# Optimization experiments

Hardware: AMD Instinct MI355X
Metric: run time of the kernel (lower is better)

The kernel has to match this reference:

```python
import jax, jax.numpy as jnp
import numpy as np

N, E, F_IN = 10000, 160000, 256
H1, C1 = 8, 128          # conv1: heads=8, out 128 per head, concat -> 1024
H2, C2 = 1, 64           # conv2: heads=1, out 64
NEG_SLOPE = 0.2


def setup_inputs() -> dict:
    key = jax.random.key(0)
    ks = jax.random.split(key, 10)
    s_in = 1.0 / np.sqrt(F_IN)
    s_h1 = 1.0 / np.sqrt(H1 * C1)
    return {
        "x": jax.random.normal(ks[0], (N, F_IN), dtype=jnp.float32),
        "edge_index": jax.random.randint(ks[1], (2, E), 0, N, dtype=jnp.int64),
        "W1": jax.random.normal(ks[2], (F_IN, H1 * C1), dtype=jnp.float32) * s_in,
        "att_src1": jax.random.normal(ks[3], (H1, C1), dtype=jnp.float32) * 0.1,
        "att_dst1": jax.random.normal(ks[4], (H1, C1), dtype=jnp.float32) * 0.1,
        "b1": jnp.zeros((H1 * C1,), dtype=jnp.float32),
        "W2": jax.random.normal(ks[5], (H1 * C1, H2 * C2), dtype=jnp.float32) * s_h1,
        "att_src2": jax.random.normal(ks[6], (H2, C2), dtype=jnp.float32) * 0.1,
        "att_dst2": jax.random.normal(ks[7], (H2, C2), dtype=jnp.float32) * 0.1,
        "b2": jnp.zeros((H2 * C2,), dtype=jnp.float32),
    }


def gat_conv(x, src, dst, W, att_src, att_dst, b, n):
    """PyG GATConv (eval mode: dropout off), concat=True, add_self_loops handled by caller."""
    H, C = att_src.shape
    h = (x @ W).reshape(n, H, C)                       # [N,H,C]
    a_s = jnp.einsum('nhc,hc->nh', h, att_src)         # [N,H]
    a_d = jnp.einsum('nhc,hc->nh', h, att_dst)         # [N,H]
    e = jax.nn.leaky_relu(a_s[src] + a_d[dst], NEG_SLOPE)  # [Etot,H]
    # softmax over edges grouped by destination node (numerically stable)
    e_max = jax.ops.segment_max(e, dst, num_segments=n)
    e = jnp.exp(e - e_max[dst])
    denom = jax.ops.segment_sum(e, dst, num_segments=n)
    alpha = e / (denom[dst] + 1e-16)                   # [Etot,H]
    msg = h[src] * alpha[:, :, None]                   # [Etot,H,C]
    out = jax.ops.segment_sum(msg, dst, num_segments=n)  # [N,H,C]
    return out.reshape(n, H * C) + b


def reference(x, edge_index, W1, att_src1, att_dst1, b1, W2, att_src2, att_dst2, b2):
    n = x.shape[0]
    loops = jnp.arange(n, dtype=edge_index.dtype)
    src = jnp.concatenate([edge_index[0], loops])
    dst = jnp.concatenate([edge_index[1], loops])
    h = jax.nn.elu(gat_conv(x, src, dst, W1, att_src1, att_dst1, b1, n))
    return gat_conv(h, src, dst, W2, att_src2, att_dst2, b2, n)
```

## Files before the change

### kernel.cpp

```cpp
#include <hip/hip_runtime.h>
#include <cmath>


typedef _Float16 f16x8 __attribute__((ext_vector_type(8)));
typedef float f32x4 __attribute__((ext_vector_type(4)));
typedef unsigned short u16x8 __attribute__((ext_vector_type(8)));

__device__ __forceinline__ float lrelu(float x) { return x > 0.f ? x : 0.2f * x; }
__device__ __forceinline__ unsigned short f2h(float f) {
  _Float16 h = (_Float16)f;
  return __builtin_bit_cast(unsigned short, h);
}
__device__ __forceinline__ float h2f(unsigned short u) {
  return (float)__builtin_bit_cast(_Float16, u);
}

__device__ __forceinline__ void fma8h(float* acc, uint4 v, float e) {
  acc[0] += e * h2f((unsigned short)(v.x & 0xffffu));
  acc[1] += e * h2f((unsigned short)(v.x >> 16));
  acc[2] += e * h2f((unsigned short)(v.y & 0xffffu));
  acc[3] += e * h2f((unsigned short)(v.y >> 16));
  acc[4] += e * h2f((unsigned short)(v.z & 0xffffu));
  acc[5] += e * h2f((unsigned short)(v.z >> 16));
  acc[6] += e * h2f((unsigned short)(v.w & 0xffffu));
  acc[7] += e * h2f((unsigned short)(v.w >> 16));
}

#define GLOAD_LDS16(gsrc, ldst)                                              \
  __builtin_amdgcn_global_load_lds(                                          \
      (const __attribute__((address_space(1))) unsigned int*)(gsrc),         \
      (__attribute__((address_space(3))) unsigned int*)(ldst), 16, 0, 0)


__global__ __launch_bounds__(256) void prep_fused(
    const int* __restrict__ ei, int* __restrict__ counts, int E,
    const float* __restrict__ x, unsigned short* __restrict__ xpk, int N, int MB1,
    const float* __restrict__ W1, unsigned short* __restrict__ w1pk,
    const float* __restrict__ W2, unsigned short* __restrict__ w2pk) {
  const int countB = (E + 255) / 256;
  const int pxB = MB1 * 8;
  int bid = blockIdx.x;
  int t = threadIdx.x;

  if (bid < countB) {
    int e = bid * 256 + t;
    if (e < E) atomicAdd(&counts[ei[E + e]], 1);
    return;
  }
  bid -= countB;
  if (bid < pxB) {
    int mb = bid >> 3, ks = bid & 7;
    int l = t & 63, f = t >> 6;
    int row = mb * 64 + f * 16 + (l & 15);
    int kc = ks * 32 + (l >> 4) * 8;
    float v[8];
#pragma unroll
    for (int j = 0; j < 8; ++j) v[j] = 0.f;
    if (row < N) {
      const float* xr = x + (size_t)row * 256 + kc;
#pragma unroll
      for (int j = 0; j < 8; ++j) v[j] = xr[j];
    }
    u16x8 hv;
#pragma unroll
    for (int j = 0; j < 8; ++j) hv[j] = f2h(v[j]);
    size_t base = (size_t)(mb * 8 + ks) * 2048;
    *(u16x8*)(xpk + base + (size_t)f * 512 + l * 8) = hv;
    return;
  }
  bid -= pxB;
  if (bid < 64) {
    int hb = bid >> 3, ks = bid & 7;
    int l = t & 63, gq = t >> 6;
    for (int g = gq; g < 8; g += 4) {
      int n = hb * 128 + g * 16 + (l & 15);
      int k0 = ks * 32 + (l >> 4) * 8;
      u16x8 hv;
#pragma unroll
      for (int j = 0; j < 8; ++j) hv[j] = f2h(W1[(size_t)(k0 + j) * 1024 + n]);
      size_t base = (size_t)(hb * 8 + ks) * 4096;
      *(u16x8*)(w1pk + base + (size_t)g * 512 + l * 8) = hv;
    }
    return;
  }
  bid -= 64;
  {
    int ks = bid;
    int l = t & 63, g = t >> 6;
    int n = g * 16 + (l & 15);
    int k0 = ks * 32 + (l >> 4) * 8;
    u16x8 hv;
#pragma unroll
    for (int j = 0; j < 8; ++j) hv[j] = f2h(W2[(size_t)(k0 + j) * 64 + n]);
    size_t base = (size_t)ks * 2048;
    *(u16x8*)(w2pk + base + (size_t)g * 512 + l * 8) = hv;
  }
}


__global__ __launch_bounds__(256) void scan_blk(const int* __restrict__ counts,
                                                int* __restrict__ offsets,
                                                int* __restrict__ bsum, int n) {
  __shared__ int lds[256];
  int b = blockIdx.x, t = threadIdx.x, i = b * 256 + t;
  int v = (i < n) ? counts[i] + 1 : 0;
  lds[t] = v;
  __syncthreads();
  for (int off = 1; off < 256; off <<= 1) {
    int tv = (t >= off) ? lds[t - off] : 0;
    __syncthreads();
    lds[t] += tv;
    __syncthreads();
  }
  if (i < n) offsets[i] = lds[t] - v;
  if (t == 255) bsum[b] = lds[255];
}

__global__ __launch_bounds__(256) void scan_apply(int* __restrict__ offsets,
                                                  int* __restrict__ cursors,
                                                  const int* __restrict__ bsum,
                                                  int nb, int n) {
  __shared__ int pre_s;
  int b = blockIdx.x, t = threadIdx.x;
  if (t == 0) {
    int s = 0;
    for (int i = 0; i < b; ++i) s += bsum[i];
    pre_s = s;
    if (b == nb - 1) {
      int tot = s;
      for (int i = b; i < nb; ++i) tot += bsum[i];
      offsets[n] = tot;
    }
  }
  __syncthreads();
  int i = b * 256 + t;
  if (i < n) {
    int o = offsets[i] + pre_s;
    offsets[i] = o;
    cursors[i] = o;
  }
}

__global__ __launch_bounds__(256) void fill_all(const int* __restrict__ ei,
                                                int* __restrict__ cursors,
                                                const int* __restrict__ offsets,
                                                int* __restrict__ list,
                                                int E, int n) {
  int tid = blockIdx.x * 256 + threadIdx.x;
  if (tid < E) {
    int d = ei[E + tid];
    int pos = atomicAdd(&cursors[d], 1);
    list[pos] = ei[tid];
  } else if (tid < E + n) {
    int i = tid - E;
    list[offsets[i + 1] - 1] = i;
  }
}


__global__ __launch_bounds__(512, 4) void gemm1_att(
    const unsigned short* __restrict__ xpk, const unsigned short* __restrict__ w1pk,
    const float* __restrict__ asrc, const float* __restrict__ adst,
    unsigned short* __restrict__ h1b, float* __restrict__ as1,
    float* __restrict__ ad1) {
  extern __shared__ char sm[];
  const int t = threadIdx.x, wid = t >> 6, lane = t & 63;
  const int wr = wid >> 2, wc = wid & 3;
  const int mb = blockIdx.x, hb = blockIdx.y;
  const int m0 = mb * 128;
  const int l15 = lane & 15, l4 = lane >> 4;

  f32x4 acc[4][2] = {};

  auto stage = [&](int buf, int ks) {
    char* base0 = sm + buf * 16384;
    for (int i = wid; i < 16; i += 8) {
      const unsigned short* src;
      int ldsoff;
      if (i < 8) {
        int r = i >> 2;
        src = xpk + (size_t)((2 * mb + r) * 8 + ks) * 2048 + (i & 3) * 512 + lane * 8;
        ldsoff = i * 1024;
      } else {
        int g = i - 8;
        src = w1pk + (size_t)(hb * 8 + ks) * 4096 + g * 512 + lane * 8;
        ldsoff = 8192 + g * 1024;
      }
      GLOAD_LDS16(src, base0 + ldsoff);
    }
  };

  stage(0, 0);
  __syncthreads();
  int buf = 0;
  for (int step = 0; step < 8; ++step) {
    if (step < 7) stage(buf ^ 1, step + 1);
    const char* b = sm + buf * 16384;
    f16x8 ah[4], bh[2];
#pragma unroll
    for (int mf = 0; mf < 4; ++mf)
      ah[mf] = *(const f16x8*)(b + (wr * 4 + mf) * 1024 + lane * 16);
#pragma unroll
    for (int nf = 0; nf < 2; ++nf)
      bh[nf] = *(const f16x8*)(b + 8192 + (wc * 2 + nf) * 1024 + lane * 16);
#pragma unroll
    for (int mf = 0; mf < 4; ++mf)
#pragma unroll
      for (int nf = 0; nf < 2; ++nf)
        acc[mf][nf] = __builtin_amdgcn_mfma_f32_16x16x32_f16(ah[mf], bh[nf], acc[mf][nf], 0, 0, 0);
    __syncthreads();
    buf ^= 1;
  }

  float* parts_s = (float*)sm;
  float* parts_d = (float*)(sm + 2048);
  unsigned short* ctile = (unsigned short*)(sm + 4096);
  float as_c[2], ad_c[2];
#pragma unroll
  for (int nf = 0; nf < 2; ++nf) {
    int col = hb * 128 + wc * 32 + nf * 16 + l15;
    as_c[nf] = asrc[col];
    ad_c[nf] = adst[col];
  }
#pragma unroll
  for (int mf = 0; mf < 4; ++mf) {
    float ss[4] = {0.f, 0.f, 0.f, 0.f}, dd[4] = {0.f, 0.f, 0.f, 0.f};
#pragma unroll
    for (int nf = 0; nf < 2; ++nf)
#pragma unroll
      for (int r = 0; r < 4; ++r) {
        ss[r] += acc[mf][nf][r] * as_c[nf];
        dd[r] += acc[mf][nf][r] * ad_c[nf];
      }
#pragma unroll
    for (int r = 0; r < 4; ++r)
      for (int m = 1; m < 16; m <<= 1) {
        ss[r] += __shfl_xor(ss[r], m);
        dd[r] += __shfl_xor(dd[r], m);
      }
    if (l15 == 0) {
#pragma unroll
      for (int r = 0; r < 4; ++r) {
        int row = wr * 64 + mf * 16 + l4 * 4 + r;
        parts_s[row * 4 + wc] = ss[r];
        parts_d[row * 4 + wc] = dd[r];
      }
    }
#pragma unroll
    for (int nf = 0; nf < 2; ++nf)
#pragma unroll
      for (int r = 0; r < 4; ++r) {
        int row = wr * 64 + mf * 16 + l4 * 4 + r;
        int col = wc * 32 + nf * 16 + l15;
        ctile[row * 128 + col] = f2h(acc[mf][nf][r]);
      }
  }
  __syncthreads();
  if (t < 128) {
    float s = parts_s[t * 4] + parts_s[t * 4 + 1] + parts_s[t * 4 + 2] + parts_s[t * 4 + 3];
    float d = parts_d[t * 4] + parts_d[t * 4 + 1] + parts_d[t * 4 + 2] + parts_d[t * 4 + 3];
    as1[(size_t)(m0 + t) * 8 + hb] = s;
    ad1[(size_t)(m0 + t) * 8 + hb] = d;
  }
#pragma unroll
  for (int rep = 0; rep < 4; ++rep) {
    int e = rep * 4096 + t * 8;
    int row = e >> 7, col = e & 127;
    u16x8 v = *(const u16x8*)(ctile + e);
    *(u16x8*)(h1b + (size_t)(m0 + row) * 1024 + hb * 128 + col) = v;
  }
}


__global__ __launch_bounds__(256) void agg1_gather(
    const unsigned short* __restrict__ h1b, const float* __restrict__ as1,
    const float* __restrict__ ad1, const int* __restrict__ offsets,
    const int* __restrict__ list, const float* __restrict__ b1,
    unsigned short* __restrict__ o1pk, int n, int nblk) {
  __shared__ __align__(16) unsigned short stg[4096];
  const int t = threadIdx.x, w = t >> 6, lane = t & 63;
  const int h0 = lane >> 4, h1_ = h0 + 4;

  for (int blk = blockIdx.x; blk < nblk; blk += gridDim.x) {
    const int node = blk * 4 + w;
    if (node < n) {
      const int beg = offsets[node], end = offsets[node + 1];
      const float ad0 = ad1[(size_t)node * 8 + h0];
      const float ad4 = ad1[(size_t)node * 8 + h1_];
      float acc0[8] = {}, acc1[8] = {};
      float den0 = 0.f, den4 = 0.f;

      int j = beg;
      int sA = 0, sB = 0;
      float aA0 = 0.f, aA4 = 0.f, aB0 = 0.f, aB4 = 0.f;
      uint4 vA0, vA1, vB0, vB1;
      if (j + 2 <= end) {
        sA = list[j]; sB = list[j + 1];
        aA0 = as1[(size_t)sA * 8 + h0]; aA4 = as1[(size_t)sA * 8 + h1_];
        aB0 = as1[(size_t)sB * 8 + h0]; aB4 = as1[(size_t)sB * 8 + h1_];
        vA0 = *(const uint4*)(h1b + (size_t)sA * 1024 + lane * 8);
        vA1 = *(const uint4*)(h1b + (size_t)sA * 1024 + 512 + lane * 8);
        vB0 = *(const uint4*)(h1b + (size_t)sB * 1024 + lane * 8);
        vB1 = *(const uint4*)(h1b + (size_t)sB * 1024 + 512 + lane * 8);
      }
      for (; j + 4 <= end; j += 2) {
        int sA2 = list[j + 2], sB2 = list[j + 3];
        float aA02 = as1[(size_t)sA2 * 8 + h0], aA42 = as1[(size_t)sA2 * 8 + h1_];
        float aB02 = as1[(size_t)sB2 * 8 + h0], aB42 = as1[(size_t)sB2 * 8 + h1_];
        uint4 nA0 = *(const uint4*)(h1b + (size_t)sA2 * 1024 + lane * 8);
        uint4 nA1 = *(const uint4*)(h1b + (size_t)sA2 * 1024 + 512 + lane * 8);
        uint4 nB0 = *(const uint4*)(h1b + (size_t)sB2 * 1024 + lane * 8);
        uint4 nB1 = *(const uint4*)(h1b + (size_t)sB2 * 1024 + 512 + lane * 8);
        float eA0 = __expf(lrelu(aA0 + ad0)), eA4 = __expf(lrelu(aA4 + ad4));
        float eB0 = __expf(lrelu(aB0 + ad0)), eB4 = __expf(lrelu(aB4 + ad4));
        den0 += eA0 + eB0; den4 += eA4 + eB4;
        fma8h(acc0, vA0, eA0); fma8h(acc1, vA1, eA4);
        fma8h(acc0, vB0, eB0); fma8h(acc1, vB1, eB4);
        sA = sA2; sB = sB2;
        aA0 = aA02; aA4 = aA42; aB0 = aB02; aB4 = aB42;
        vA0 = nA0; vA1 = nA1; vB0 = nB0; vB1 = nB1;
      }
      if (j + 2 <= end) {
        float eA0 = __expf(lrelu(aA0 + ad0)), eA4 = __expf(lrelu(aA4 + ad4));
        float eB0 = __expf(lrelu(aB0 + ad0)), eB4 = __expf(lrelu(aB4 + ad4));
        den0 += eA0 + eB0; den4 += eA4 + eB4;
        fma8h(acc0, vA0, eA0); fma8h(acc1, vA1, eA4);
        fma8h(acc0, vB0, eB0); fma8h(acc1, vB1, eB4);
        j += 2;
      }
      if (j < end) {
        int s = list[j];
        float a0 = as1[(size_t)s * 8 + h0], a4 = as1[(size_t)s * 8 + h1_];
        uint4 v0 = *(const uint4*)(h1b + (size_t)s * 1024 + lane * 8);
        uint4 v1 = *(const uint4*)(h1b + (size_t)s * 1024 + 512 + lane * 8);
        float e0 = __expf(lrelu(a0 + ad0)), e4 = __expf(lrelu(a4 + ad4));
        den0 += e0; den4 += e4;
        fma8h(acc0, v0, e0); fma8h(acc1, v1, e4);
      }

      const float inv0 = 1.f / (den0 + 1e-16f);
      const float inv4 = 1.f / (den4 + 1e-16f);
      u16x8 hA8, hB8;
#pragma unroll
      for (int k = 0; k < 8; ++k) {
        float vA = acc0[k] * inv0 + b1[lane * 8 + k];
        float vB = acc1[k] * inv4 + b1[512 + lane * 8 + k];
        vA = vA > 0.f ? vA : expm1f(vA);
        vB = vB > 0.f ? vB : expm1f(vB);
        hA8[k] = f2h(vA);
        hB8[k] = f2h(vB);
      }
      const int q2 = lane >> 2, kc = lane & 3;
      {
        int aw = q2 * 256 + kc * 64 + w * 16;
        *(u16x8*)((char*)stg + (aw ^ ((q2 & 7) << 4))) = hA8;
      }
      {
        int ks = 16 + q2;
        int aw = ks * 256 + kc * 64 + w * 16;
        *(u16x8*)((char*)stg + (aw ^ ((ks & 7) << 4))) = hB8;
      }
    }
    __syncthreads();
    const int mb = blk >> 4, f = (blk >> 2) & 3, l15b = (blk & 3) * 4;
#pragma unroll
    for (int it = 0; it < 2; ++it) {
      int a = it * 4096 + t * 16;
      int ks = a >> 8, kcc = (a >> 6) & 3, ww = (a >> 4) & 3;
      u16x8 v = *(const u16x8*)((const char*)stg + (a ^ ((ks & 7) << 4)));
      size_t g = (size_t)(mb * 32 + ks) * 2048 + (size_t)f * 512 +
                 (size_t)(kcc * 16 + l15b + ww) * 8;
      *(u16x8*)(o1pk + g) = v;
    }
    __syncthreads();
  }
}


__global__ __launch_bounds__(256) void gemm2_splitk(
    const unsigned short* __restrict__ o1pk, const unsigned short* __restrict__ w2pk,
    float* __restrict__ h2p, int Mpad) {
  extern __shared__ char sm[];
  const int t = threadIdx.x, wid = t >> 6, lane = t & 63;
  const int wr = wid >> 1, wc = wid & 1;
  const int mb = blockIdx.x, sk = blockIdx.y;
  const int m0 = mb * 64;
  const int l15 = lane & 15, l4 = lane >> 4;

  f32x4 acc[2][2] = {};

  auto stage = [&](int buf, int ks) {
    char* base0 = sm + buf * 8192;
    const unsigned short* ax = o1pk + (size_t)(mb * 32 + ks) * 2048 + lane * 8;
    for (int i = wid; i < 4; i += 4)
      GLOAD_LDS16(ax + i * 512, base0 + i * 1024);
    if (wid >= 0) {
      int i = wid;
      GLOAD_LDS16(ax + i * 512, base0 + i * 1024);
      const unsigned short* bw = w2pk + (size_t)ks * 2048 + lane * 8;
      GLOAD_LDS16(bw + i * 512, base0 + 4096 + i * 1024);
    }
  };

  stage(0, sk * 8);
  __syncthreads();
  int buf = 0;
  for (int step = 0; step < 8; ++step) {
    if (step < 7) stage(buf ^ 1, sk * 8 + step + 1);
    const char* b = sm + buf * 8192;
    f16x8 ah[2], bh[2];
#pragma unroll
    for (int mf = 0; mf < 2; ++mf)
      ah[mf] = *(const f16x8*)(b + (wr * 2 + mf) * 1024 + lane * 16);
#pragma unroll
    for (int nf = 0; nf < 2; ++nf)
      bh[nf] = *(const f16x8*)(b + 4096 + (wc * 2 + nf) * 1024 + lane * 16);
#pragma unroll
    for (int mf = 0; mf < 2; ++mf)
#pragma unroll
      for (int nf = 0; nf < 2; ++nf)
        acc[mf][nf] = __builtin_amdgcn_mfma_f32_16x16x32_f16(ah[mf], bh[nf], acc[mf][nf], 0, 0, 0);
    __syncthreads();
    buf ^= 1;
  }

#pragma unroll
  for (int mf = 0; mf < 2; ++mf)
#pragma unroll
    for (int nf = 0; nf < 2; ++nf)
#pragma unroll
      for (int r = 0; r < 4; ++r) {
        int row = wr * 32 + mf * 16 + l4 * 4 + r;
        int col = wc * 32 + nf * 16 + l15;
        h2p[((size_t)sk * Mpad + m0 + row) * 64 + col] = acc[mf][nf][r];
      }
}


__global__ __launch_bounds__(256) void reduce_att2(
    const float* __restrict__ h2p, const float* __restrict__ asrc,
    const float* __restrict__ adst, float* __restrict__ h2,
    float* __restrict__ as2, float* __restrict__ ad2, int Mpad, int n) {
  int w = threadIdx.x >> 6, lane = threadIdx.x & 63;
  int row = blockIdx.x * 4 + w;
  if (row >= n) return;
  float s = 0.f;
#pragma unroll
  for (int sk = 0; sk < 4; ++sk) s += h2p[((size_t)sk * Mpad + row) * 64 + lane];
  h2[(size_t)row * 64 + lane] = s;
  float ds = s * asrc[lane], dd = s * adst[lane];
  for (int o = 32; o; o >>= 1) { ds += __shfl_xor(ds, o); dd += __shfl_xor(dd, o); }
  if (lane == 0) { as2[row] = ds; ad2[row] = dd; }
}


__global__ __launch_bounds__(256) void agg2_gather(
    const float* __restrict__ h2, const float* __restrict__ as2,
    const float* __restrict__ ad2, const int* __restrict__ offsets,
    const int* __restrict__ list, const float* __restrict__ b2,
    float* __restrict__ out, int n, int nblk) {
  const int wid = threadIdx.x >> 6, lane = threadIdx.x & 63;
  const int cb = (lane & 15) * 4;
  const int jo = lane >> 4;

  for (int blk = blockIdx.x; blk < nblk; blk += gridDim.x) {
    const int node = blk * 4 + wid;
    if (node >= n) continue;
    const int beg = offsets[node], end = offsets[node + 1];
    const float ad = ad2[node];

    float4 acc = make_float4(0.f, 0.f, 0.f, 0.f);
    float den = 0.f;
    for (int j = beg + jo; j < end; j += 4) {
      int s = list[j];
      float e = __expf(lrelu(as2[s] + ad));
      den += e;
      float4 v = *(const float4*)&h2[(size_t)s * 64 + cb];
      acc.x += e * v.x; acc.y += e * v.y; acc.z += e * v.z; acc.w += e * v.w;
    }
    acc.x += __shfl_xor(acc.x, 16); acc.y += __shfl_xor(acc.y, 16);
    acc.z += __shfl_xor(acc.z, 16); acc.w += __shfl_xor(acc.w, 16);
    den += __shfl_xor(den, 16);
    acc.x += __shfl_xor(acc.x, 32); acc.y += __shfl_xor(acc.y, 32);
    acc.z += __shfl_xor(acc.z, 32); acc.w += __shfl_xor(acc.w, 32);
    den += __shfl_xor(den, 32);
    if (jo == 0) {
      float inv = 1.f / (den + 1e-16f);
      float4 r;
      r.x = acc.x * inv + b2[cb];
      r.y = acc.y * inv + b2[cb + 1];
      r.z = acc.z * inv + b2[cb + 2];
      r.w = acc.w * inv + b2[cb + 3];
      *(float4*)&out[(size_t)node * 64 + cb] = r;
    }
  }
}


extern "C" void kernel_launch(void* const* d_in, const int* in_sizes, int n_in,
                              void* d_out, int out_size, void* d_ws, size_t ws_size,
                              hipStream_t stream) {
  const float* x     = (const float*)d_in[0];
  const int*   ei    = (const int*)d_in[1];
  const float* W1    = (const float*)d_in[2];
  const float* asrc1 = (const float*)d_in[3];
  const float* adst1 = (const float*)d_in[4];
  const float* b1    = (const float*)d_in[5];
  const float* W2    = (const float*)d_in[6];
  const float* asrc2 = (const float*)d_in[7];
  const float* adst2 = (const float*)d_in[8];
  const float* b2    = (const float*)d_in[9];
  float* out = (float*)d_out;

  const int N = in_sizes[0] / 256;
  const int E = in_sizes[1] / 2;
  const int T = E + N;
  const int MBB = (N + 127) / 128;
  const int Mpad = MBB * 128;
  const int MB1 = Mpad / 64;
  const int NB = (N + 255) / 256;
  const int NBLK4 = (N + 3) / 4;
  const int AGG_GRID = NBLK4 < 2048 ? NBLK4 : 2048;

  char* p = (char*)d_ws;
  auto bump = [&](size_t bytes) {
    char* r = p;
    p += (bytes + 255) & ~(size_t)255;
    return r;
  };
  int* counts  = (int*)bump((size_t)N * 4);
  int* offsets = (int*)bump((size_t)(N + 1) * 4);
  int* cursors = (int*)bump((size_t)N * 4);
  int* bsum    = (int*)bump((size_t)NB * 4);
  int* list    = (int*)bump((size_t)T * 4);
  unsigned short* xpk  = (unsigned short*)bump((size_t)Mpad * 256 * 2);
  unsigned short* w1pk = (unsigned short*)bump((size_t)1024 * 256 * 2);
  unsigned short* h1b  = (unsigned short*)bump((size_t)Mpad * 1024 * 2);
  float* as1           = (float*)bump((size_t)Mpad * 8 * 4);
  float* ad1           = (float*)bump((size_t)Mpad * 8 * 4);
  unsigned short* o1pk = (unsigned short*)bump((size_t)Mpad * 1024 * 2);
  unsigned short* w2pk = (unsigned short*)bump((size_t)64 * 1024 * 2);
  float* as2           = (float*)bump((size_t)Mpad * 4);
  float* ad2           = (float*)bump((size_t)Mpad * 4);
  float* h2p = (float*)h1b;
  float* h2  = (float*)xpk;

  hipMemsetAsync(counts, 0, (size_t)N * 4, stream);
  {
    int gridsz = (E + 255) / 256 + MB1 * 8 + 64 + 32;
    prep_fused<<<gridsz, 256, 0, stream>>>(ei, counts, E, x, xpk, N, MB1,
                                           W1, w1pk, W2, w2pk);
  }
  scan_blk<<<NB, 256, 0, stream>>>(counts, offsets, bsum, N);
  scan_apply<<<NB, 256, 0, stream>>>(offsets, cursors, bsum, NB, N);
  fill_all<<<(E + N + 255) / 256, 256, 0, stream>>>(ei, cursors, offsets, list, E, N);

  gemm1_att<<<dim3(MBB, 8), 512, 36864, stream>>>(xpk, w1pk, asrc1, adst1, h1b, as1, ad1);
  agg1_gather<<<AGG_GRID, 256, 0, stream>>>(h1b, as1, ad1, offsets, list, b1, o1pk, N, NBLK4);

  gemm2_splitk<<<dim3(Mpad / 64, 4), 256, 16384, stream>>>(o1pk, w2pk, h2p, Mpad);
  reduce_att2<<<(N + 3) / 4, 256, 0, stream>>>(h2p, asrc2, adst2, h2, as2, ad2, Mpad, N);
  agg2_gather<<<AGG_GRID, 256, 0, stream>>>(h2, as2, ad2, offsets, list, b2, out, N, NBLK4);
}
```

Baseline: 145.4 us.

## Split layer-1 aggregation per head with edge-parallel quads and shuffle reduction

```diff
diff --git a/kernel.cpp b/kernel.cpp
--- a/kernel.cpp
+++ b/kernel.cpp
@@ -276,103 +276,66 @@
     const unsigned short* __restrict__ h1b, const float* __restrict__ as1,
     const float* __restrict__ ad1, const int* __restrict__ offsets,
     const int* __restrict__ list, const float* __restrict__ b1,
-    unsigned short* __restrict__ o1pk, int n, int nblk) {
-  __shared__ __align__(16) unsigned short stg[4096];
-  const int t = threadIdx.x, w = t >> 6, lane = t & 63;
-  const int h0 = lane >> 4, h1_ = h0 + 4;
-
-  for (int blk = blockIdx.x; blk < nblk; blk += gridDim.x) {
-    const int node = blk * 4 + w;
-    if (node < n) {
-      const int beg = offsets[node], end = offsets[node + 1];
-      const float ad0 = ad1[(size_t)node * 8 + h0];
-      const float ad4 = ad1[(size_t)node * 8 + h1_];
-      float acc0[8] = {}, acc1[8] = {};
-      float den0 = 0.f, den4 = 0.f;
-
-      int j = beg;
-      int sA = 0, sB = 0;
-      float aA0 = 0.f, aA4 = 0.f, aB0 = 0.f, aB4 = 0.f;
-      uint4 vA0, vA1, vB0, vB1;
-      if (j + 2 <= end) {
-        sA = list[j]; sB = list[j + 1];
-        aA0 = as1[(size_t)sA * 8 + h0]; aA4 = as1[(size_t)sA * 8 + h1_];
-        aB0 = as1[(size_t)sB * 8 + h0]; aB4 = as1[(size_t)sB * 8 + h1_];
-        vA0 = *(const uint4*)(h1b + (size_t)sA * 1024 + lane * 8);
-        vA1 = *(const uint4*)(h1b + (size_t)sA * 1024 + 512 + lane * 8);
-        vB0 = *(const uint4*)(h1b + (size_t)sB * 1024 + lane * 8);
-        vB1 = *(const uint4*)(h1b + (size_t)sB * 1024 + 512 + lane * 8);
-      }
-      for (; j + 4 <= end; j += 2) {
-        int sA2 = list[j + 2], sB2 = list[j + 3];
-        float aA02 = as1[(size_t)sA2 * 8 + h0], aA42 = as1[(size_t)sA2 * 8 + h1_];
-        float aB02 = as1[(size_t)sB2 * 8 + h0], aB42 = as1[(size_t)sB2 * 8 + h1_];
-        uint4 nA0 = *(const uint4*)(h1b + (size_t)sA2 * 1024 + lane * 8);
-        uint4 nA1 = *(const uint4*)(h1b + (size_t)sA2 * 1024 + 512 + lane * 8);
-        uint4 nB0 = *(const uint4*)(h1b + (size_t)sB2 * 1024 + lane * 8);
-        uint4 nB1 = *(const uint4*)(h1b + (size_t)sB2 * 1024 + 512 + lane * 8);
-        float eA0 = __expf(lrelu(aA0 + ad0)), eA4 = __expf(lrelu(aA4 + ad4));
-        float eB0 = __expf(lrelu(aB0 + ad0)), eB4 = __expf(lrelu(aB4 + ad4));
-        den0 += eA0 + eB0; den4 += eA4 + eB4;
-        fma8h(acc0, vA0, eA0); fma8h(acc1, vA1, eA4);
-        fma8h(acc0, vB0, eB0); fma8h(acc1, vB1, eB4);
-        sA = sA2; sB = sB2;
-        aA0 = aA02; aA4 = aA42; aB0 = aB02; aB4 = aB42;
-        vA0 = nA0; vA1 = nA1; vB0 = nB0; vB1 = nB1;
-      }
-      if (j + 2 <= end) {
-        float eA0 = __expf(lrelu(aA0 + ad0)), eA4 = __expf(lrelu(aA4 + ad4));
-        float eB0 = __expf(lrelu(aB0 + ad0)), eB4 = __expf(lrelu(aB4 + ad4));
-        den0 += eA0 + eB0; den4 += eA4 + eB4;
-        fma8h(acc0, vA0, eA0); fma8h(acc1, vA1, eA4);
-        fma8h(acc0, vB0, eB0); fma8h(acc1, vB1, eB4);
-        j += 2;
-      }
-      if (j < end) {
-        int s = list[j];
-        float a0 = as1[(size_t)s * 8 + h0], a4 = as1[(size_t)s * 8 + h1_];
-        uint4 v0 = *(const uint4*)(h1b + (size_t)s * 1024 + lane * 8);
-        uint4 v1 = *(const uint4*)(h1b + (size_t)s * 1024 + 512 + lane * 8);
-        float e0 = __expf(lrelu(a0 + ad0)), e4 = __expf(lrelu(a4 + ad4));
-        den0 += e0; den4 += e4;
-        fma8h(acc0, v0, e0); fma8h(acc1, v1, e4);
-      }
-
-      const float inv0 = 1.f / (den0 + 1e-16f);
-      const float inv4 = 1.f / (den4 + 1e-16f);
-      u16x8 hA8, hB8;
+    unsigned short* __restrict__ o1pk, int n, int nitems) {
+  const int w = threadIdx.x >> 6, lane = threadIdx.x & 63;
+  const int quad = lane >> 4, li = lane & 15;
+
+  for (int item = blockIdx.x; item < nitems; item += gridDim.x) {
+    const int c = item & 7;
+    const int q = item >> 3;
+    const int node = q * 4 + w;
+    if (node >= n) continue;
+    const int beg = offsets[node], end = offsets[node + 1];
+    const float adc = ad1[(size_t)node * 8 + c];
+    const unsigned short* hrow = h1b + (size_t)c * 128 + (size_t)li * 8;
+
+    float acc[8] = {};
+    float den = 0.f;
+    int j = beg + quad;
+    int s0 = 0;
+    float a0 = 0.f;
+    uint4 v0 = make_uint4(0, 0, 0, 0);
+    if (j < end) {
+      s0 = list[j];
+      a0 = as1[(size_t)s0 * 8 + c];
+      v0 = *(const uint4*)(hrow + (size_t)s0 * 1024);
+    }
+    for (; j + 4 < end; j += 4) {
+      int s1 = list[j + 4];
+      float a1 = as1[(size_t)s1 * 8 + c];
+      uint4 v1 = *(const uint4*)(hrow + (size_t)s1 * 1024);
+      float e = __expf(lrelu(a0 + adc));
+      den += e;
+      fma8h(acc, v0, e);
+      s0 = s1; a0 = a1; v0 = v1;
+    }
+    if (j < end) {
+      float e = __expf(lrelu(a0 + adc));
+      den += e;
+      fma8h(acc, v0, e);
+    }
+#pragma unroll
+    for (int k = 0; k < 8; ++k) {
+      acc[k] += __shfl_xor(acc[k], 16);
+      acc[k] += __shfl_xor(acc[k], 32);
+    }
+    den += __shfl_xor(den, 16);
+    den += __shfl_xor(den, 32);
+    if (quad == 0) {
+      float inv = 1.f / (den + 1e-16f);
+      u16x8 hv;
 #pragma unroll
       for (int k = 0; k < 8; ++k) {
-        float vA = acc0[k] * inv0 + b1[lane * 8 + k];
-        float vB = acc1[k] * inv4 + b1[512 + lane * 8 + k];
-        vA = vA > 0.f ? vA : expm1f(vA);
-        vB = vB > 0.f ? vB : expm1f(vB);
-        hA8[k] = f2h(vA);
-        hB8[k] = f2h(vB);
-      }
-      const int q2 = lane >> 2, kc = lane & 3;
-      {
-        int aw = q2 * 256 + kc * 64 + w * 16;
-        *(u16x8*)((char*)stg + (aw ^ ((q2 & 7) << 4))) = hA8;
-      }
-      {
-        int ks = 16 + q2;
-        int aw = ks * 256 + kc * 64 + w * 16;
-        *(u16x8*)((char*)stg + (aw ^ ((ks & 7) << 4))) = hB8;
-      }
-    }
-    __syncthreads();
-    const int mb = blk >> 4, f = (blk >> 2) & 3, l15b = (blk & 3) * 4;
-#pragma unroll
-    for (int it = 0; it < 2; ++it) {
-      int a = it * 4096 + t * 16;
-      int ks = a >> 8, kcc = (a >> 6) & 3, ww = (a >> 4) & 3;
-      u16x8 v = *(const u16x8*)((const char*)stg + (a ^ ((ks & 7) << 4)));
+        float v = acc[k] * inv + b1[c * 128 + li * 8 + k];
+        v = v > 0.f ? v : expm1f(v);
+        hv[k] = f2h(v);
+      }
+      int mb = node >> 6, f = (node >> 4) & 3, l15n = node & 15;
+      int ks = 4 * c + (li >> 2), kc = li & 3;
       size_t g = (size_t)(mb * 32 + ks) * 2048 + (size_t)f * 512 +
-                 (size_t)(kcc * 16 + l15b + ww) * 8;
-      *(u16x8*)(o1pk + g) = v;
-    }
-    __syncthreads();
+                 (size_t)(kc * 16 + l15n) * 8;
+      *(u16x8*)(o1pk + g) = hv;
+    }
   }
 }
 
@@ -392,14 +355,9 @@
   auto stage = [&](int buf, int ks) {
     char* base0 = sm + buf * 8192;
     const unsigned short* ax = o1pk + (size_t)(mb * 32 + ks) * 2048 + lane * 8;
-    for (int i = wid; i < 4; i += 4)
-      GLOAD_LDS16(ax + i * 512, base0 + i * 1024);
-    if (wid >= 0) {
-      int i = wid;
-      GLOAD_LDS16(ax + i * 512, base0 + i * 1024);
-      const unsigned short* bw = w2pk + (size_t)ks * 2048 + lane * 8;
-      GLOAD_LDS16(bw + i * 512, base0 + 4096 + i * 1024);
-    }
+    const unsigned short* bw = w2pk + (size_t)ks * 2048 + lane * 8;
+    GLOAD_LDS16(ax + wid * 512, base0 + wid * 1024);
+    GLOAD_LDS16(bw + wid * 512, base0 + 4096 + wid * 1024);
   };
 
   stage(0, sk * 8);
@@ -520,7 +478,9 @@
   const int MB1 = Mpad / 64;
   const int NB = (N + 255) / 256;
   const int NBLK4 = (N + 3) / 4;
-  const int AGG_GRID = NBLK4 < 2048 ? NBLK4 : 2048;
+  const int NITEMS1 = NBLK4 * 8;
+  const int AGG1_GRID = NITEMS1 < 2048 ? NITEMS1 : 2048;
+  const int AGG2_GRID = NBLK4 < 2048 ? NBLK4 : 2048;
 
   char* p = (char*)d_ws;
   auto bump = [&](size_t bytes) {
@@ -556,9 +516,9 @@
   fill_all<<<(E + N + 255) / 256, 256, 0, stream>>>(ei, cursors, offsets, list, E, N);
 
   gemm1_att<<<dim3(MBB, 8), 512, 36864, stream>>>(xpk, w1pk, asrc1, adst1, h1b, as1, ad1);
-  agg1_gather<<<AGG_GRID, 256, 0, stream>>>(h1b, as1, ad1, offsets, list, b1, o1pk, N, NBLK4);
+  agg1_gather<<<AGG1_GRID, 256, 0, stream>>>(h1b, as1, ad1, offsets, list, b1, o1pk, N, NITEMS1);
 
   gemm2_splitk<<<dim3(Mpad / 64, 4), 256, 16384, stream>>>(o1pk, w2pk, h2p, Mpad);
   reduce_att2<<<(N + 3) / 4, 256, 0, stream>>>(h2p, asrc2, adst2, h2, as2, ad2, Mpad, N);
-  agg2_gather<<<AGG_GRID, 256, 0, stream>>>(h2, as2, ad2, offsets, list, b2, out, N, NBLK4);
-}
+  agg2_gather<<<AGG2_GRID, 256, 0, stream>>>(h2, as2, ad2, offsets, list, b2, out, N, NBLK4);
+}
```

Measured after the change: 146.2 us. No clear change (+0.5%).
